# Optimization experiments

Hardware: AMD Instinct MI355X
Metric: run time of the kernel (lower is better)

Reference implementation:

```python
import jax, jax.numpy as jnp
import numpy as np

B, S, D, H, L, V = 2, 2048, 1024, 16, 4, 2000
DK = D // H
DFF = 4 * D
EPS = 1e-5


def _pos_encoding(s, d):
    pos = np.arange(s, dtype=np.float64)[:, None]
    i = np.arange(d, dtype=np.float64)[None, :]
    angle = pos / np.power(10000.0, (i - (i % 2)) / d)
    pe = np.where(i % 2 == 0, np.sin(angle), np.cos(angle))
    return jnp.asarray(pe, jnp.float32)  # [S, D]


def setup_inputs() -> dict:
    key = jax.random.key(0)
    ks = jax.random.split(key, 12)
    sc = 0.02
    return {
        "indices": jax.random.randint(ks[0], (B, S), 0, V),
        "emb": jax.random.normal(ks[1], (V, D), jnp.float32) * sc,
        "Wq": jax.random.normal(ks[2], (L, H, DK, D), jnp.float32) * sc,
        "Wk": jax.random.normal(ks[3], (L, H, DK, D), jnp.float32) * sc,
        "Wv": jax.random.normal(ks[4], (L, H, DK, D), jnp.float32) * sc,
        "Wo": jax.random.normal(ks[5], (L, D, D), jnp.float32) * sc,
        "ln1_w": jnp.ones((L, D), jnp.float32),
        "ln1_b": jnp.zeros((L, D), jnp.float32),
        "W1": jax.random.normal(ks[6], (L, DFF, D), jnp.float32) * sc,
        "W2": jax.random.normal(ks[7], (L, D, DFF), jnp.float32) * sc,
        "ln2_w": jnp.ones((L, D), jnp.float32),
        "ln2_b": jnp.zeros((L, D), jnp.float32),
        "Wout": jax.random.normal(ks[8], (V, D), jnp.float32) * sc,
    }


def _layernorm(x, w, b):
    m = jnp.mean(x, axis=-1, keepdims=True)
    v = jnp.mean(jnp.square(x - m), axis=-1, keepdims=True)
    return (x - m) * jax.lax.rsqrt(v + EPS) * w + b


def reference(indices, emb, Wq, Wk, Wv, Wo, ln1_w, ln1_b, W1, W2, ln2_w, ln2_b, Wout):
    x = emb[indices] + _pos_encoding(S, D)  # [B, S, D]
    causal = jnp.tril(jnp.ones((S, S), bool))
    inv_sqrt_dk = 1.0 / np.sqrt(DK)
    for l in range(L):
        # per-head QKV projections, vectorized over heads
        q = jnp.einsum("bsd,hkd->bhsk", x, Wq[l])
        k = jnp.einsum("bsd,hkd->bhsk", x, Wk[l])
        v = jnp.einsum("bsd,hkd->bhsk", x, Wv[l])
        scores = jnp.einsum("bhqk,bhmk->bhqm", q, k) * inv_sqrt_dk
        scores = jnp.where(causal, scores, -jnp.inf)
        attn = jax.nn.softmax(scores, axis=-1)
        o = jnp.einsum("bhqm,bhmk->bhqk", attn, v)
        o = o.transpose(0, 2, 1, 3).reshape(B, S, D)  # concat heads
        o = o @ Wo[l].T
        x = _layernorm(x + o, ln1_w[l], ln1_b[l])
        h = jax.nn.relu(x @ W1[l].T) @ W2[l].T
        x = _layernorm(x + h, ln2_w[l], ln2_b[l])
    return x @ Wout.T  # [B, S, V]
```

## Files before the change

### kernel.cpp

```cpp
#include <hip/hip_runtime.h>
#include <hip/hip_bf16.h>

#define B_   2
#define S_   2048
#define D_   1024
#define H_   16
#define L_   4
#define DK_  64
#define DFF_ 4096
#define V_   2000

typedef __bf16 bf16x8 __attribute__((ext_vector_type(8)));
typedef float  f32x4  __attribute__((ext_vector_type(4)));
typedef __attribute__((address_space(1))) const void* as1cv;
typedef __attribute__((address_space(3))) void* as3v;

__device__ __forceinline__ void async_copy16(const void* g, void* l) {
    __builtin_amdgcn_global_load_lds((as1cv)g, (as3v)l, 16, 0, 0);
}

__global__ __launch_bounds__(256)
void canon_k(const void* __restrict__ src, __hip_bfloat16* __restrict__ dst,
             long n, const unsigned short* __restrict__ probe)
{
    const bool isbf = (probe[0] == 0x3F80u);
    long i0 = ((long)blockIdx.x * 256 + threadIdx.x) * 8;
    if (isbf) {
        const __hip_bfloat16* s = (const __hip_bfloat16*)src;
        #pragma unroll
        for (int j = 0; j < 8; ++j) {
            long i = i0 + j;
            if (i < n) dst[i] = s[i];
        }
    } else {
        const float* s = (const float*)src;
        #pragma unroll
        for (int j = 0; j < 8; ++j) {
            long i = i0 + j;
            if (i < n) dst[i] = __float2bfloat16(s[i]);
        }
    }
}

template<int MODE>
__global__ __launch_bounds__(256, 2)
void gemm_bt(const __hip_bfloat16* __restrict__ A,
             const __hip_bfloat16* __restrict__ Wa,
             const __hip_bfloat16* __restrict__ Wb,
             const __hip_bfloat16* __restrict__ Wc,
             void* __restrict__ Oa, void* __restrict__ Obp, void* __restrict__ Ocp,
             const __hip_bfloat16* __restrict__ Res,
             const unsigned short* __restrict__ probe,
             int M, int N, int K)
{
    const __hip_bfloat16* W = Wa;
    void* Out = Oa;
    if (blockIdx.z == 1) { W = Wb; Out = Obp; }
    else if (blockIdx.z == 2) { W = Wc; Out = Ocp; }

    __shared__ __bf16 As[128 * 32];
    __shared__ __bf16 Bs[128 * 32];

    const int tid  = threadIdx.x;
    const int wave = tid >> 6;
    const int lane = tid & 63;
    const int quad = lane >> 4;
    const int l16  = lane & 15;
    const int bm = blockIdx.x;
    const int bn = blockIdx.y;
    const int wm = (wave >> 1) * 64;
    const int wn = (wave & 1) * 64;

    const int sr = tid >> 2;
    const int sc = (tid & 3) * 8;
    const __hip_bfloat16* ap0 = A + (long)(bm * 128 + sr) * K + sc;
    const __hip_bfloat16* ap1 = ap0 + (long)64 * K;
    const __hip_bfloat16* bp0 = W + (long)(bn * 128 + sr) * K + sc;
    const __hip_bfloat16* bp1 = bp0 + (long)64 * K;
    const bool bok0 = (bn * 128 + sr) < N;
    const bool bok1 = (bn * 128 + sr + 64) < N;

    __bf16* aL0 = As + wave * 512;
    __bf16* aL1 = As + 2048 + wave * 512;
    __bf16* bL0 = Bs + wave * 512;
    __bf16* bL1 = Bs + 2048 + wave * 512;

    if (N & 127) {
        #pragma unroll
        for (int j = 0; j < 2; ++j)
            *(bf16x8*)(Bs + (j * 256 + tid) * 8) = (bf16x8)0;
        __syncthreads();
    }

    f32x4 acc[4][4] = {};

    for (int k0 = 0; k0 < K; k0 += 32) {
        async_copy16(ap0 + k0, aL0);
        async_copy16(ap1 + k0, aL1);
        if (bok0) async_copy16(bp0 + k0, bL0);
        if (bok1) async_copy16(bp1 + k0, bL1);
        __syncthreads();

        bf16x8 af[4], bfr[4];
        #pragma unroll
        for (int i = 0; i < 4; ++i)
            af[i] = *(const bf16x8*)(As + (wm + i * 16 + l16) * 32 + quad * 8);
        #pragma unroll
        for (int i = 0; i < 4; ++i)
            bfr[i] = *(const bf16x8*)(Bs + (wn + i * 16 + l16) * 32 + quad * 8);
        #pragma unroll
        for (int i = 0; i < 4; ++i)
            #pragma unroll
            for (int j = 0; j < 4; ++j)
                acc[i][j] = __builtin_amdgcn_mfma_f32_16x16x32_bf16(af[i], bfr[j], acc[i][j], 0, 0, 0);
        __syncthreads();
    }

    const bool out_bf = (MODE != 1) && (MODE != 3 || probe[0] == 0x3F80u);
    #pragma unroll
    for (int i = 0; i < 4; ++i) {
        #pragma unroll
        for (int r = 0; r < 4; ++r) {
            const long row = bm * 128 + wm + i * 16 + quad * 4 + r;
            #pragma unroll
            for (int j = 0; j < 4; ++j) {
                const int col = bn * 128 + wn + j * 16 + l16;
                if (col < N) {
                    const long idx = row * (long)N + col;
                    float v = acc[i][j][r];
                    if constexpr (MODE == 1) {
                        ((float*)Out)[idx] = v + __bfloat162float(Res[idx]);
                    } else if constexpr (MODE == 2) {
                        ((__hip_bfloat16*)Out)[idx] = __float2bfloat16(v > 0.f ? v : 0.f);
                    } else {
                        if (out_bf) ((__hip_bfloat16*)Out)[idx] = __float2bfloat16(v);
                        else        ((float*)Out)[idx] = v;
                    }
                }
            }
        }
    }
}

__global__ __launch_bounds__(256, 2)
void flash_attn(const __hip_bfloat16* __restrict__ Qg,
                const __hip_bfloat16* __restrict__ Kg,
                const __hip_bfloat16* __restrict__ Vg,
                __hip_bfloat16* __restrict__ Og)
{
    const int h  = blockIdx.y;
    const int b  = blockIdx.z;
    const int tid  = threadIdx.x;
    const int wave = tid >> 6;
    const int lane = tid & 63;
    const int quad = lane >> 4;
    const int l16  = lane & 15;

    __shared__ __bf16 Qs[64 * 64];
    __shared__ __bf16 Ks[64 * 64];
    __shared__ __bf16 Vs[64 * 64];
    __shared__ __bf16 Vt[64 * 72];
    __shared__ __bf16 Ps[4][16 * 72];

    const long base = ((long)b * S_) * D_ + (long)h * DK_;
    const int sr  = tid >> 3;
    const int scq = ((tid & 7) ^ (sr & 7)) * 8;
    const int scv = (tid & 7) * 8;

    const float scale = 0.125f;

    for (int pr = 0; pr < 2; ++pr) {
        const int qt = pr ? (31 - (int)blockIdx.x) : (int)blockIdx.x;

        const __hip_bfloat16* qp = Qg + base + (long)(qt * 64 + sr) * D_ + scq;
        async_copy16(qp,           Qs + wave * 512);
        async_copy16(qp + 32 * D_, Qs + 2048 + wave * 512);
        __syncthreads();

        const int qr = wave * 16 + l16;
        const __bf16* qrow = Qs + qr * 64;
        const bf16x8 qf0 = *(const bf16x8*)(qrow + (( quad      ^ (qr & 7)) * 8));
        const bf16x8 qf1 = *(const bf16x8*)(qrow + (((quad + 4) ^ (qr & 7)) * 8));

        f32x4 o_acc[4] = {};
        float m_run[4], l_run[4];
        #pragma unroll
        for (int r = 0; r < 4; ++r) { m_run[r] = -1e30f; l_run[r] = 0.f; }

        const int q_base = qt * 64 + wave * 16 + quad * 4;

        for (int kv0 = 0; kv0 <= qt * 64; kv0 += 64) {
            const __hip_bfloat16* kp = Kg + base + (long)(kv0 + sr) * D_ + scq;
            const __hip_bfloat16* vp = Vg + base + (long)(kv0 + sr) * D_ + scv;
            async_copy16(kp,           Ks + wave * 512);
            async_copy16(kp + 32 * D_, Ks + 2048 + wave * 512);
            async_copy16(vp,           Vs + wave * 512);
            async_copy16(vp + 32 * D_, Vs + 2048 + wave * 512);
            __syncthreads();

            #pragma unroll
            for (int i = 0; i < 2; ++i) {
                const int seg = i * 256 + tid;
                const int dk  = seg & 63;
                const int kvc = (seg >> 6) * 8;
                bf16x8 t;
                #pragma unroll
                for (int j = 0; j < 8; ++j) t[j] = Vs[(kvc + j) * 64 + dk];
                *(bf16x8*)(Vt + dk * 72 + kvc) = t;
            }
            __syncthreads();

            f32x4 sAcc[4] = {};
            #pragma unroll
            for (int nt = 0; nt < 4; ++nt) {
                const int kr = nt * 16 + l16;
                const __bf16* krow = Ks + kr * 64;
                const bf16x8 kf0 = *(const bf16x8*)(krow + (( quad      ^ (kr & 7)) * 8));
                const bf16x8 kf1 = *(const bf16x8*)(krow + (((quad + 4) ^ (kr & 7)) * 8));
                sAcc[nt] = __builtin_amdgcn_mfma_f32_16x16x32_bf16(qf0, kf0, sAcc[nt], 0, 0, 0);
                sAcc[nt] = __builtin_amdgcn_mfma_f32_16x16x32_bf16(qf1, kf1, sAcc[nt], 0, 0, 0);
            }

            const bool diag = (kv0 == qt * 64);
            float rmax[4];
            #pragma unroll
            for (int r = 0; r < 4; ++r) rmax[r] = -1e30f;
            #pragma unroll
            for (int nt = 0; nt < 4; ++nt)
                #pragma unroll
                for (int r = 0; r < 4; ++r) {
                    float s = sAcc[nt][r] * scale;
                    if (diag && (kv0 + nt * 16 + l16) > (q_base + r)) s = -1e30f;
                    sAcc[nt][r] = s;
                    rmax[r] = fmaxf(rmax[r], s);
                }
            #pragma unroll
            for (int off = 1; off < 16; off <<= 1)
                #pragma unroll
                for (int r = 0; r < 4; ++r)
                    rmax[r] = fmaxf(rmax[r], __shfl_xor(rmax[r], off, 64));

            float alpha[4], rsum[4];
            #pragma unroll
            for (int r = 0; r < 4; ++r) {
                const float mn = fmaxf(m_run[r], rmax[r]);
                alpha[r] = __expf(m_run[r] - mn);
                m_run[r] = mn;
                rsum[r] = 0.f;
            }
            #pragma unroll
            for (int nt = 0; nt < 4; ++nt)
                #pragma unroll
                for (int r = 0; r < 4; ++r) {
                    const float p = __expf(sAcc[nt][r] - m_run[r]);
                    sAcc[nt][r] = p;
                    rsum[r] += p;
                }
            #pragma unroll
            for (int off = 1; off < 16; off <<= 1)
                #pragma unroll
                for (int r = 0; r < 4; ++r)
                    rsum[r] += __shfl_xor(rsum[r], off, 64);
            #pragma unroll
            for (int r = 0; r < 4; ++r) l_run[r] = l_run[r] * alpha[r] + rsum[r];
            #pragma unroll
            for (int nt = 0; nt < 4; ++nt)
                #pragma unroll
                for (int r = 0; r < 4; ++r) o_acc[nt][r] *= alpha[r];

            __bf16* pw = &Ps[wave][0];
            #pragma unroll
            for (int nt = 0; nt < 4; ++nt)
                #pragma unroll
                for (int r = 0; r < 4; ++r)
                    pw[(quad * 4 + r) * 72 + nt * 16 + l16] = (__bf16)sAcc[nt][r];
            __syncthreads();
            const __bf16* pb = pw + l16 * 72 + quad * 8;
            const bf16x8 pf0 = *(const bf16x8*)pb;
            const bf16x8 pf1 = *(const bf16x8*)(pb + 32);
            #pragma unroll
            for (int nt = 0; nt < 4; ++nt) {
                const __bf16* vb = Vt + (nt * 16 + l16) * 72 + quad * 8;
                o_acc[nt] = __builtin_amdgcn_mfma_f32_16x16x32_bf16(pf0, *(const bf16x8*)vb,        o_acc[nt], 0, 0, 0);
                o_acc[nt] = __builtin_amdgcn_mfma_f32_16x16x32_bf16(pf1, *(const bf16x8*)(vb + 32), o_acc[nt], 0, 0, 0);
            }
            __syncthreads();
        }

        #pragma unroll
        for (int nt = 0; nt < 4; ++nt)
            #pragma unroll
            for (int r = 0; r < 4; ++r) {
                const long row = (long)b * S_ + qt * 64 + wave * 16 + quad * 4 + r;
                const int col = h * DK_ + nt * 16 + l16;
                Og[row * D_ + col] = __float2bfloat16(o_acc[nt][r] / l_run[r]);
            }
    }
}

__global__ __launch_bounds__(256)
void layernorm_k(const float* __restrict__ in,
                 const __hip_bfloat16* __restrict__ w,
                 const __hip_bfloat16* __restrict__ bb,
                 __hip_bfloat16* __restrict__ out)
{
    const int row = blockIdx.x;
    const int tid = threadIdx.x;
    const float4 v = ((const float4*)(in + (long)row * D_))[tid];
    float s  = v.x + v.y + v.z + v.w;
    float ss = v.x * v.x + v.y * v.y + v.z * v.z + v.w * v.w;
    #pragma unroll
    for (int off = 1; off < 64; off <<= 1) {
        s  += __shfl_xor(s, off, 64);
        ss += __shfl_xor(ss, off, 64);
    }
    __shared__ float red[8];
    if ((tid & 63) == 0) { red[tid >> 6] = s; red[4 + (tid >> 6)] = ss; }
    __syncthreads();
    s  = red[0] + red[1] + red[2] + red[3];
    ss = red[4] + red[5] + red[6] + red[7];
    const float mean = s * (1.f / D_);
    const float var  = ss * (1.f / D_) - mean * mean;
    const float rs = rsqrtf(var + 1e-5f);
    const int d0 = tid * 4;
    const float xs[4] = { v.x, v.y, v.z, v.w };
    #pragma unroll
    for (int j = 0; j < 4; ++j) {
        const float wv = __bfloat162float(w[d0 + j]);
        const float bv = __bfloat162float(bb[d0 + j]);
        out[(long)row * D_ + d0 + j] = __float2bfloat16((xs[j] - mean) * rs * wv + bv);
    }
}

__global__ __launch_bounds__(256)
void embed_k(const int* __restrict__ idx,
             const __hip_bfloat16* __restrict__ emb,
             __hip_bfloat16* __restrict__ X)
{
    const int row = blockIdx.x;
    const int s = row & (S_ - 1);
    const int tid = threadIdx.x;
    const int token = idx[row];
    const __hip_bfloat16* e = emb + (long)token * D_;
    #pragma unroll
    for (int j = 0; j < 4; ++j) {
        const int d = tid + j * 256;
        const float di = (float)(d & ~1);
        const float freq = __expf(di * (-9.210340371976184f / (float)D_));
        const float angle = (float)s * freq;
        const float pe = (d & 1) ? cosf(angle) : sinf(angle);
        X[(long)row * D_ + d] = __float2bfloat16(__bfloat162float(e[d]) + pe);
    }
}

extern "C" void kernel_launch(void* const* d_in, const int* in_sizes, int n_in,
                              void* d_out, int out_size, void* d_ws, size_t ws_size,
                              hipStream_t stream)
{
    const int* indices = (const int*)d_in[0];
    const unsigned short* probe = (const unsigned short*)d_in[6];

    const long NTOK = (long)B_ * S_;
    char* ws = (char*)d_ws;
    __hip_bfloat16* X  = (__hip_bfloat16*)ws; ws += NTOK * D_ * 2;
    __hip_bfloat16* Qb = (__hip_bfloat16*)ws; ws += NTOK * D_ * 2;
    __hip_bfloat16* Kb = (__hip_bfloat16*)ws; ws += NTOK * D_ * 2;
    __hip_bfloat16* Vb = (__hip_bfloat16*)ws; ws += NTOK * D_ * 2;
    __hip_bfloat16* Ob = (__hip_bfloat16*)ws; ws += NTOK * D_ * 2;
    __hip_bfloat16* Hb = Qb;
    float* tmp = (float*)ws;                  ws += NTOK * D_ * 4;
    __hip_bfloat16* cEmb  = (__hip_bfloat16*)ws; ws += (long)V_ * D_ * 2;
    __hip_bfloat16* cWq   = (__hip_bfloat16*)ws; ws += (long)L_ * D_ * D_ * 2;
    __hip_bfloat16* cWk   = (__hip_bfloat16*)ws; ws += (long)L_ * D_ * D_ * 2;
    __hip_bfloat16* cWv   = (__hip_bfloat16*)ws; ws += (long)L_ * D_ * D_ * 2;
    __hip_bfloat16* cWo   = (__hip_bfloat16*)ws; ws += (long)L_ * D_ * D_ * 2;
    __hip_bfloat16* cW1   = (__hip_bfloat16*)ws; ws += (long)L_ * DFF_ * D_ * 2;
    __hip_bfloat16* cW2   = (__hip_bfloat16*)ws; ws += (long)L_ * D_ * DFF_ * 2;
    __hip_bfloat16* cWout = (__hip_bfloat16*)ws; ws += (long)V_ * D_ * 2;
    __hip_bfloat16* cLn1w = (__hip_bfloat16*)ws; ws += (long)L_ * D_ * 2;
    __hip_bfloat16* cLn1b = (__hip_bfloat16*)ws; ws += (long)L_ * D_ * 2;
    __hip_bfloat16* cLn2w = (__hip_bfloat16*)ws; ws += (long)L_ * D_ * 2;
    __hip_bfloat16* cLn2b = (__hip_bfloat16*)ws; ws += (long)L_ * D_ * 2;

    struct { const void* src; __hip_bfloat16* dst; long n; } cv[12] = {
        { d_in[1],  cEmb,  (long)V_ * D_ },
        { d_in[2],  cWq,   (long)L_ * D_ * D_ },
        { d_in[3],  cWk,   (long)L_ * D_ * D_ },
        { d_in[4],  cWv,   (long)L_ * D_ * D_ },
        { d_in[5],  cWo,   (long)L_ * D_ * D_ },
        { d_in[6],  cLn1w, (long)L_ * D_ },
        { d_in[7],  cLn1b, (long)L_ * D_ },
        { d_in[8],  cW1,   (long)L_ * DFF_ * D_ },
        { d_in[9],  cW2,   (long)L_ * D_ * DFF_ },
        { d_in[10], cLn2w, (long)L_ * D_ },
        { d_in[11], cLn2b, (long)L_ * D_ },
        { d_in[12], cWout, (long)V_ * D_ },
    };
    for (int i = 0; i < 12; ++i) {
        const long blocks = (cv[i].n + 2047) / 2048;
        canon_k<<<dim3((unsigned)blocks), 256, 0, stream>>>(cv[i].src, cv[i].dst, cv[i].n, probe);
    }

    embed_k<<<dim3(NTOK), 256, 0, stream>>>(indices, cEmb, X);

    for (int l = 0; l < L_; ++l) {
        const __hip_bfloat16* wq = cWq + (long)l * D_ * D_;
        const __hip_bfloat16* wk = cWk + (long)l * D_ * D_;
        const __hip_bfloat16* wv = cWv + (long)l * D_ * D_;
        const __hip_bfloat16* wo = cWo + (long)l * D_ * D_;
        const __hip_bfloat16* w1 = cW1 + (long)l * DFF_ * D_;
        const __hip_bfloat16* w2 = cW2 + (long)l * D_ * DFF_;

        gemm_bt<0><<<dim3(32, 8, 3), 256, 0, stream>>>(X, wq, wk, wv, Qb, Kb, Vb, nullptr, nullptr, 4096, 1024, 1024);
        flash_attn<<<dim3(16, 16, 2), 256, 0, stream>>>(Qb, Kb, Vb, Ob);
        gemm_bt<1><<<dim3(32, 8, 1), 256, 0, stream>>>(Ob, wo, wo, wo, tmp, tmp, tmp, X, nullptr, 4096, 1024, 1024);
        layernorm_k<<<dim3(4096), 256, 0, stream>>>(tmp, cLn1w + l * D_, cLn1b + l * D_, X);
        gemm_bt<2><<<dim3(32, 32, 1), 256, 0, stream>>>(X, w1, w1, w1, Hb, Hb, Hb, nullptr, nullptr, 4096, 4096, 1024);
        gemm_bt<1><<<dim3(32, 8, 1), 256, 0, stream>>>(Hb, w2, w2, w2, tmp, tmp, tmp, X, nullptr, 4096, 1024, 4096);
        layernorm_k<<<dim3(4096), 256, 0, stream>>>(tmp, cLn2w + l * D_, cLn2b + l * D_, X);
    }

    gemm_bt<3><<<dim3(32, 16, 1), 256, 0, stream>>>(X, cWout, cWout, cWout, d_out, d_out, d_out, nullptr, probe, 4096, V_, 1024);
}
```

Before: 1.607 ms.

## Double-buffer LDS tiles in GEMM to overlap global loads with MFMA

Adds a second shared-memory buffer for the A and B tiles. The loop now issues the asynchronous global-to-LDS copy for step k+1 before running the MFMAs on step k, and keeps a single barrier per iteration. The aim is to hide global load latency behind compute instead of stalling at a barrier after each load. LDS use doubles to 32KB per block, which may limit occupancy with launch bounds of 2 blocks per CU. A single barrier may also not be enough to wait for the async copies to finish.

```diff
diff --git a/kernel.cpp b/kernel.cpp
--- a/kernel.cpp
+++ b/kernel.cpp
@@ -58,8 +58,8 @@
     if (blockIdx.z == 1) { W = Wb; Out = Obp; }
     else if (blockIdx.z == 2) { W = Wc; Out = Ocp; }
 
-    __shared__ __bf16 As[128 * 32];
-    __shared__ __bf16 Bs[128 * 32];
+    __shared__ __bf16 As[2][128 * 32];
+    __shared__ __bf16 Bs[2][128 * 32];
 
     const int tid  = threadIdx.x;
     const int wave = tid >> 6;
@@ -80,40 +80,50 @@
     const bool bok0 = (bn * 128 + sr) < N;
     const bool bok1 = (bn * 128 + sr + 64) < N;
 
-    __bf16* aL0 = As + wave * 512;
-    __bf16* aL1 = As + 2048 + wave * 512;
-    __bf16* bL0 = Bs + wave * 512;
-    __bf16* bL1 = Bs + 2048 + wave * 512;
-
     if (N & 127) {
         #pragma unroll
-        for (int j = 0; j < 2; ++j)
-            *(bf16x8*)(Bs + (j * 256 + tid) * 8) = (bf16x8)0;
+        for (int bi = 0; bi < 2; ++bi)
+            #pragma unroll
+            for (int j = 0; j < 2; ++j)
+                *(bf16x8*)(Bs[bi] + (j * 256 + tid) * 8) = (bf16x8)0;
         __syncthreads();
     }
 
     f32x4 acc[4][4] = {};
-
-    for (int k0 = 0; k0 < K; k0 += 32) {
-        async_copy16(ap0 + k0, aL0);
-        async_copy16(ap1 + k0, aL1);
-        if (bok0) async_copy16(bp0 + k0, bL0);
-        if (bok1) async_copy16(bp1 + k0, bL1);
-        __syncthreads();
+    const int nsteps = K >> 5;
+
+    async_copy16(ap0, As[0] + wave * 512);
+    async_copy16(ap1, As[0] + 2048 + wave * 512);
+    if (bok0) async_copy16(bp0, Bs[0] + wave * 512);
+    if (bok1) async_copy16(bp1, Bs[0] + 2048 + wave * 512);
+    __syncthreads();
+
+    int cur = 0;
+    for (int t = 0; t < nsteps; ++t) {
+        const int nxt = cur ^ 1;
+        if (t + 1 < nsteps) {
+            const int k0 = (t + 1) << 5;
+            async_copy16(ap0 + k0, As[nxt] + wave * 512);
+            async_copy16(ap1 + k0, As[nxt] + 2048 + wave * 512);
+            if (bok0) async_copy16(bp0 + k0, Bs[nxt] + wave * 512);
+            if (bok1) async_copy16(bp1 + k0, Bs[nxt] + 2048 + wave * 512);
+        }
 
         bf16x8 af[4], bfr[4];
         #pragma unroll
         for (int i = 0; i < 4; ++i)
-            af[i] = *(const bf16x8*)(As + (wm + i * 16 + l16) * 32 + quad * 8);
+            af[i] = *(const bf16x8*)(As[cur] + (wm + i * 16 + l16) * 32 + quad * 8);
         #pragma unroll
         for (int i = 0; i < 4; ++i)
-            bfr[i] = *(const bf16x8*)(Bs + (wn + i * 16 + l16) * 32 + quad * 8);
+            bfr[i] = *(const bf16x8*)(Bs[cur] + (wn + i * 16 + l16) * 32 + quad * 8);
         #pragma unroll
         for (int i = 0; i < 4; ++i)
             #pragma unroll
             for (int j = 0; j < 4; ++j)
                 acc[i][j] = __builtin_amdgcn_mfma_f32_16x16x32_bf16(af[i], bfr[j], acc[i][j], 0, 0, 0);
+
         __syncthreads();
+        cur = nxt;
     }
 
     const bool out_bf = (MODE != 1) && (MODE != 3 || probe[0] == 0x3F80u);
```

Result: no change. 1.615 ms (+0.5%).
